# Optimization experiments

Hardware: AMD Instinct MI355X
Metric: run time of the kernel (lower is better)

Reference implementation:

```python
import jax, jax.numpy as jnp
import numpy as np
from jax import lax

NPOINT, RADIUS, NSAMPLE = 1024, 0.2, 32
EPS = 1e-5

def _fps(xyz, npoint):
    # farthest point sampling, xyz [B,N,3] -> idx [B,npoint]
    B, N, _ = xyz.shape
    def body(carry, _):
        dist, far = carry  # [B,N], [B]
        c = jnp.take_along_axis(xyz, far[:, None, None], axis=1)  # [B,1,3]
        d = jnp.sum((xyz - c) ** 2, -1)
        dist = jnp.minimum(dist, d)
        nxt = jnp.argmax(dist, -1).astype(jnp.int32)
        return (dist, nxt), far
    init = (jnp.full((B, N), 1e10, xyz.dtype), jnp.zeros((B,), jnp.int32))
    _, idx = lax.scan(body, init, None, length=npoint)
    return jnp.transpose(idx)  # [B,npoint]

def _index_points(pts, idx):
    # pts [B,N,C], idx [B,...] int -> [B,...,C]
    return jax.vmap(lambda p, i: p[i])(pts, idx)

def _ball_query(radius, nsample, xyz, new_xyz):
    B, N, _ = xyz.shape
    sqr = (jnp.sum(new_xyz ** 2, -1)[:, :, None] + jnp.sum(xyz ** 2, -1)[:, None, :]
           - 2.0 * jnp.einsum('bsc,bnc->bsn', new_xyz, xyz))  # [B,S,N]
    base = jnp.arange(N, dtype=jnp.int32)[None, None, :]
    idx = jnp.where(sqr > radius ** 2, N, base)
    idx = jnp.sort(idx, -1)[..., :nsample]  # [B,S,K]
    first = idx[..., :1]
    return jnp.where(idx == N, jnp.broadcast_to(first, idx.shape), idx)

def _mlp_bn_relu(x, w, b, g, beta):
    # x [B,C,K,S]; 1x1 conv == channel GEMM; BN uses batch stats (training mode)
    x = jnp.einsum('bcks,oc->boks', x, w) + b[None, :, None, None]
    mu = jnp.mean(x, axis=(0, 2, 3), keepdims=True)
    var = jnp.var(x, axis=(0, 2, 3), keepdims=True)
    x = (x - mu) * lax.rsqrt(var + EPS) * g[None, :, None, None] + beta[None, :, None, None]
    return jax.nn.relu(x)

def setup_inputs() -> dict:
    key = jax.random.key(0)
    ks = jax.random.split(key, 16)
    B, N, D = 16, 4096, 3
    mlp = [64, 64, 128]
    inp = {
        'xyz': jax.random.uniform(ks[0], (B, 3, N), jnp.float32),
        'features': jax.random.normal(ks[1], (B, D, N), jnp.float32),
    }
    last = 3 + D
    for i, c in enumerate(mlp):
        inp[f'w{i}'] = jax.random.normal(ks[2 + 4 * i], (c, last), jnp.float32) * (1.0 / np.sqrt(last))
        inp[f'b{i}'] = jnp.zeros((c,), jnp.float32)
        inp[f'g{i}'] = jnp.ones((c,), jnp.float32)
        inp[f'bt{i}'] = jnp.zeros((c,), jnp.float32)
        last = c
    return inp

def reference(xyz, features, w0, b0, g0, bt0, w1, b1, g1, bt1, w2, b2, g2, bt2):
    xyz_t = jnp.transpose(xyz, (0, 2, 1))        # [B,N,3]
    feat_t = jnp.transpose(features, (0, 2, 1))  # [B,N,D]
    fps_idx = _fps(xyz_t, NPOINT)
    new_xyz = _index_points(xyz_t, fps_idx)      # [B,S,3]
    idx = _ball_query(RADIUS, NSAMPLE, xyz_t, new_xyz)  # [B,S,K]
    grouped_xyz = _index_points(xyz_t, idx) - new_xyz[:, :, None, :]  # [B,S,K,3]
    grouped_feat = _index_points(feat_t, idx)                          # [B,S,K,D]
    x = jnp.concatenate([grouped_xyz, grouped_feat], -1)               # [B,S,K,3+D]
    x = jnp.transpose(x, (0, 3, 2, 1))           # [B,C,K,S]
    for (w, b, g, beta) in ((w0, b0, g0, bt0), (w1, b1, g1, bt1), (w2, b2, g2, bt2)):
        x = _mlp_bn_relu(x, w, b, g, beta)
    new_features = jnp.max(x, axis=2)            # [B,C',S]
    return jnp.transpose(new_xyz, (0, 2, 1)), new_features
```

## Files before the change

kernel.cpp:

```cpp
#include <hip/hip_runtime.h>
#include <hip/hip_bf16.h>
#include <stdint.h>

#define NB 16
#define NPTS 4096
#define NS 1024
#define NK 32
#define NT_COLS (NB*NS*NK)
#define NBUCK 64

typedef __hip_bfloat16 bf16;
typedef __attribute__((ext_vector_type(8))) short short8;
typedef __attribute__((ext_vector_type(4))) float floatx4;

__device__ __forceinline__ unsigned short f2bf_bits(float v) {
  bf16 b = __float2bfloat16(v);
  return *(unsigned short*)&b;
}

__global__ void k_zero(float* __restrict__ p) {
  p[blockIdx.x*256 + threadIdx.x] = 0.f;
}

template<int CTRL, int RM, int BM>
__device__ __forceinline__ float fmax_dpp(float x) {
  int o = __builtin_amdgcn_update_dpp(__float_as_int(x), __float_as_int(x),
                                      CTRL, RM, BM, false);
  return fmaxf(x, __int_as_float(o));
}
template<int CTRL>
__device__ __forceinline__ float add_dpp(float x) {
  int o = __builtin_amdgcn_update_dpp(0, __float_as_int(x), CTRL, 0xF, 0xF, true);
  return __fadd_rn(x, __int_as_float(o));
}

__global__ __launch_bounds__(256) void k_fps(const float* __restrict__ xyz,
                                             float* __restrict__ newxyz,
                                             float* __restrict__ out0) {
  __shared__ float xs[NPTS], ys[NPTS], zs[NPTS];
  __shared__ float selx[NS], sely[NS], selz[NS];
  __shared__ float2 pair[2][4];
  const int b = blockIdx.x;
  const int t = threadIdx.x;
  const float* p = xyz + (size_t)b * 3 * NPTS;
  for (int i = t; i < NPTS; i += 256) {
    xs[i] = p[i];
    ys[i] = p[NPTS + i];
    zs[i] = p[2*NPTS + i];
  }
  __syncthreads();
  float px[16], py[16], pz[16], dist[16];
  const int p0 = t * 16;
  #pragma unroll
  for (int j = 0; j < 16; ++j) {
    px[j]=xs[p0+j]; py[j]=ys[p0+j]; pz[j]=zs[p0+j]; dist[j]=1e10f;
  }
  const int lane = t & 63, wv = t >> 6;
  int cur = 0;
  for (int i = 0; i < NS; ++i) {
    float cx = xs[cur], cy = ys[cur], cz = zs[cur];
    if (t == 0) { selx[i] = cx; sely[i] = cy; selz[i] = cz; }
    if (i == NS-1) break;
    float bv = -1.0f; int bi = p0;
    #pragma unroll
    for (int j = 0; j < 16; ++j) {
      float dx = __fsub_rn(px[j], cx);
      float dy = __fsub_rn(py[j], cy);
      float dz = __fsub_rn(pz[j], cz);
      float d  = __fadd_rn(__fadd_rn(__fmul_rn(dx,dx), __fmul_rn(dy,dy)), __fmul_rn(dz,dz));
      float nd = fminf(dist[j], d);
      dist[j] = nd;
      if (nd > bv) { bv = nd; bi = p0 + j; }
    }
    float x = bv;
    x = fmax_dpp<0x111,0xF,0xF>(x);
    x = fmax_dpp<0x112,0xF,0xF>(x);
    x = fmax_dpp<0x114,0xF,0xF>(x);
    x = fmax_dpp<0x118,0xF,0xF>(x);
    x = fmax_dpp<0x142,0xA,0xF>(x);
    x = fmax_dpp<0x143,0xC,0xF>(x);
    float M = __int_as_float(__builtin_amdgcn_readlane(__float_as_int(x), 63));
    unsigned long long mk = __ballot(bv == M);
    int sl  = (int)__builtin_ctzll(mk);
    int wbi = __builtin_amdgcn_readlane(bi, sl);
    if ((t & 63) == 0) pair[i & 1][wv] = make_float2(M, __int_as_float(wbi));
    __syncthreads();
    const float4* pb = (const float4*)&pair[i & 1][0];
    float4 q01 = pb[0], q23 = pb[1];
    float bestv = q01.x; int besti = __float_as_int(q01.y);
    if (q01.z > bestv) { bestv = q01.z; besti = __float_as_int(q01.w); }
    if (q23.x > bestv) { bestv = q23.x; besti = __float_as_int(q23.y); }
    if (q23.z > bestv) { bestv = q23.z; besti = __float_as_int(q23.w); }
    cur = besti;
  }
  __syncthreads();
  for (int i = t; i < NS; i += 256) {
    float vx = selx[i], vy = sely[i], vz = selz[i];
    size_t q = (size_t)b*3*NS + i;
    out0[q] = vx; out0[q + NS] = vy; out0[q + 2*NS] = vz;
    size_t o = (size_t)(b*NS + i)*3;
    newxyz[o] = vx; newxyz[o+1] = vy; newxyz[o+2] = vz;
  }
}

__global__ __launch_bounds__(256) void k_ballq(const float* __restrict__ xyz,
                                               const float* __restrict__ newxyz,
                                               int* __restrict__ idx) {
  const int gw = (blockIdx.x * 256 + threadIdx.x) >> 6;
  const int lane = threadIdx.x & 63;
  const int b = gw >> 10;
  const int s = gw & (NS-1);
  const float* xb = xyz + (size_t)b * 3 * NPTS;
  const size_t nq = (size_t)(b*NS + s)*3;
  const float nx = newxyz[nq], ny = newxyz[nq+1], nz = newxyz[nq+2];
  const float sn = __fadd_rn(__fadd_rn(__fmul_rn(nx,nx), __fmul_rn(ny,ny)), __fmul_rn(nz,nz));
  const float R2 = (float)(0.2*0.2);
  int* out = idx + (size_t)gw * NK;
  int cnt = 0, first = 0;
  for (int c0 = 0; c0 < NPTS; c0 += 64) {
    int n = c0 + lane;
    float x = xb[n], y = xb[NPTS+n], z = xb[2*NPTS+n];
    float sx = __fadd_rn(__fadd_rn(__fmul_rn(x,x), __fmul_rn(y,y)), __fmul_rn(z,z));
    float dt = __fadd_rn(__fadd_rn(__fmul_rn(nx,x), __fmul_rn(ny,y)), __fmul_rn(nz,z));
    float sqr = __fsub_rn(__fadd_rn(sn, sx), __fmul_rn(2.0f, dt));
    bool inr = (sqr <= R2);
    unsigned long long m = __ballot(inr);
    if (m != 0ull) {
      if (cnt == 0) first = c0 + (int)__builtin_ctzll(m);
      int rank = __popcll(m & ((1ull << lane) - 1ull));
      int pos = cnt + rank;
      if (inr && pos < NK) out[pos] = n;
      cnt += __popcll(m);
      if (cnt >= NK) break;
    }
  }
  int tot = cnt < NK ? cnt : NK;
  if (lane >= tot && lane < NK) out[lane] = first;
}

__global__ __launch_bounds__(256) void k_layer1(const float* __restrict__ xyz,
                                                const float* __restrict__ feat,
                                                const float* __restrict__ newxyz,
                                                const int* __restrict__ idx,
                                                const float* __restrict__ w0,
                                                const float* __restrict__ b0,
                                                bf16* __restrict__ x1) {
  __shared__ float w[64*6];
  __shared__ float bias[64];
  for (int i = threadIdx.x; i < 64*6; i += 256) w[i] = w0[i];
  if (threadIdx.x < 64) bias[threadIdx.x] = b0[threadIdx.x];
  __syncthreads();
  const int col = blockIdx.x * 256 + threadIdx.x;
  const int bs = col >> 5;
  const int b  = bs >> 10;
  const int n  = idx[col];
  const float* xb = xyz  + (size_t)b*3*NPTS;
  const float* fb = feat + (size_t)b*3*NPTS;
  float in[6];
  in[0] = __fsub_rn(xb[n],        newxyz[(size_t)bs*3]);
  in[1] = __fsub_rn(xb[NPTS+n],   newxyz[(size_t)bs*3+1]);
  in[2] = __fsub_rn(xb[2*NPTS+n], newxyz[(size_t)bs*3+2]);
  in[3] = fb[n];
  in[4] = fb[NPTS+n];
  in[5] = fb[2*NPTS+n];
  #pragma unroll
  for (int o = 0; o < 64; ++o) {
    float acc = bias[o];
    #pragma unroll
    for (int c = 0; c < 6; ++c) acc = fmaf(in[c], w[o*6+c], acc);
    x1[(size_t)o*NT_COLS + col] = __float2bfloat16(acc);
  }
}

__global__ __launch_bounds__(256) void k_stats(const bf16* __restrict__ x,
                                               float* __restrict__ accum, int C) {
  const int o = blockIdx.x >> 5;
  const int chunk = blockIdx.x & 31;
  const uint4* p = (const uint4*)(x + (size_t)o*NT_COLS + (size_t)chunk*16384);
  float s = 0.f, ss = 0.f;
  #pragma unroll
  for (int it = 0; it < 8; ++it) {
    uint4 u = p[threadIdx.x + it*256];
    uint32_t wr[4] = {u.x, u.y, u.z, u.w};
    #pragma unroll
    for (int q = 0; q < 4; ++q) {
      float a  = __uint_as_float(wr[q] << 16);
      float bq = __uint_as_float(wr[q] & 0xffff0000u);
      s += a;  ss = fmaf(a, a, ss);
      s += bq; ss = fmaf(bq, bq, ss);
    }
  }
  #pragma unroll
  for (int off = 32; off; off >>= 1) { s += __shfl_xor(s, off); ss += __shfl_xor(ss, off); }
  __shared__ float ls[4], lss[4];
  const int lane = threadIdx.x & 63, wv = threadIdx.x >> 6;
  if (lane == 0) { ls[wv] = s; lss[wv] = ss; }
  __syncthreads();
  if (threadIdx.x == 0) {
    float* dst = accum + (size_t)(blockIdx.x & (NBUCK-1))*(2*C);
    atomicAdd(&dst[o],     (ls[0]+ls[1])+(ls[2]+ls[3]));
    atomicAdd(&dst[C + o], (lss[0]+lss[1])+(lss[2]+lss[3]));
  }
}

__global__ void k_finalize(const float* __restrict__ accum,
                           const float* __restrict__ g, const float* __restrict__ beta,
                           float* __restrict__ scsh, int C) {
  int o = threadIdx.x;
  if (o < C) {
    float s = 0.f, ss = 0.f;
    for (int bkt = 0; bkt < NBUCK; ++bkt) {
      s  += accum[(size_t)bkt*(2*C) + o];
      ss += accum[(size_t)bkt*(2*C) + C + o];
    }
    const float n = (float)NT_COLS;
    float mu  = s / n;
    float var = ss / n - mu*mu;
    if (var < 0.f) var = 0.f;
    float rs = rsqrtf(var + 1e-5f);
    float sc = g[o] * rs;
    scsh[o]   = sc;
    scsh[C+o] = beta[o] - mu * sc;
  }
}

#define XT_STRIDE 72
template<int CO, bool POOL>
__global__ __launch_bounds__(256) void k_layerN_mfma(
    const bf16*  __restrict__ xin,
    const float* __restrict__ wN,
    const float* __restrict__ bN,
    const float* __restrict__ scsh,
    float*       __restrict__ accum,
    bf16*        __restrict__ xout,
    float*       __restrict__ mx) {
  constexpr int RT = CO/16;
  __shared__ short xT[256*XT_STRIDE];
  __shared__ float sc_s[64], sh_s[64], bias_s[CO];
  const int t = threadIdx.x;
  const int col0 = blockIdx.x * 256;
  if (t < 64) { sc_s[t] = scsh[t]; sh_s[t] = scsh[64+t]; }
  if (t < CO) bias_s[t] = bN[t];
  __syncthreads();
  {
    const int col = col0 + t;
    #pragma unroll
    for (int c0 = 0; c0 < 64; c0 += 8) {
      short8 pk;
      #pragma unroll
      for (int j = 0; j < 8; ++j) {
        float v = __bfloat162float(xin[(size_t)(c0+j)*NT_COLS + col]);
        v = fmaxf(fmaf(v, sc_s[c0+j], sh_s[c0+j]), 0.f);
        pk[j] = (short)f2bf_bits(v);
      }
      *((short8*)&xT[t*XT_STRIDE + c0]) = pk;
    }
  }
  __syncthreads();
  const int lane = t & 63, wv = t >> 6;
  const int qd = lane >> 4, ln = lane & 15;
  short8 A[RT][2];
  #pragma unroll
  for (int rt = 0; rt < RT; ++rt) {
    #pragma unroll
    for (int kh = 0; kh < 2; ++kh) {
      const float* wp = wN + (size_t)(rt*16 + ln)*64 + kh*32 + qd*8;
      float4 f0 = *(const float4*)wp;
      float4 f1 = *(const float4*)(wp + 4);
      short8 a;
      a[0]=(short)f2bf_bits(f0.x); a[1]=(short)f2bf_bits(f0.y);
      a[2]=(short)f2bf_bits(f0.z); a[3]=(short)f2bf_bits(f0.w);
      a[4]=(short)f2bf_bits(f1.x); a[5]=(short)f2bf_bits(f1.y);
      a[6]=(short)f2bf_bits(f1.z); a[7]=(short)f2bf_bits(f1.w);
      A[rt][kh] = a;
    }
  }
  floatx4 acc[RT][4];
  #pragma unroll
  for (int rt = 0; rt < RT; ++rt)
    #pragma unroll
    for (int ct = 0; ct < 4; ++ct)
      acc[rt][ct] = (floatx4)0.f;
  #pragma unroll
  for (int ct = 0; ct < 4; ++ct) {
    const int coll = wv*64 + ct*16 + ln;
    short8 B0 = *((const short8*)&xT[coll*XT_STRIDE + qd*8]);
    short8 B1 = *((const short8*)&xT[coll*XT_STRIDE + 32 + qd*8]);
    #pragma unroll
    for (int rt = 0; rt < RT; ++rt) {
      acc[rt][ct] = __builtin_amdgcn_mfma_f32_16x16x32_bf16(A[rt][0], B0, acc[rt][ct], 0,0,0);
      acc[rt][ct] = __builtin_amdgcn_mfma_f32_16x16x32_bf16(A[rt][1], B1, acc[rt][ct], 0,0,0);
    }
  }
  float* dst = accum + (size_t)(blockIdx.x & (NBUCK-1))*(2*CO);
  const int bs0 = (col0 + wv*64) >> 5;
  #pragma unroll
  for (int rt = 0; rt < RT; ++rt) {
    float s[4]  = {0.f,0.f,0.f,0.f};
    float sq[4] = {0.f,0.f,0.f,0.f};
    float mxv[2][4];
    #pragma unroll
    for (int h = 0; h < 2; ++h)
      #pragma unroll
      for (int r = 0; r < 4; ++r) mxv[h][r] = -3.402823466e38f;
    #pragma unroll
    for (int ct = 0; ct < 4; ++ct) {
      const int col = col0 + wv*64 + ct*16 + ln;
      #pragma unroll
      for (int r = 0; r < 4; ++r) {
        const int o = rt*16 + qd*4 + r;
        float v = acc[rt][ct][r] + bias_s[o];
        if (!POOL) xout[(size_t)o*NT_COLS + col] = __float2bfloat16(v);
        else mxv[ct>>1][r] = fmaxf(mxv[ct>>1][r], v);
        s[r] += v; sq[r] = fmaf(v, v, sq[r]);
      }
    }
    if (POOL) {
      #pragma unroll
      for (int h = 0; h < 2; ++h) {
        #pragma unroll
        for (int r = 0; r < 4; ++r) {
          float m = mxv[h][r];
          m = fmax_dpp<0x111,0xF,0xF>(m);
          m = fmax_dpp<0x112,0xF,0xF>(m);
          m = fmax_dpp<0x114,0xF,0xF>(m);
          m = fmax_dpp<0x118,0xF,0xF>(m);
          if (ln == 15) {
            const int o = rt*16 + qd*4 + r;
            mx[(size_t)o*(NT_COLS/NK) + bs0 + h] = m;
          }
        }
      }
    }
    #pragma unroll
    for (int r = 0; r < 4; ++r) {
      float a = s[r], q = sq[r];
      a = add_dpp<0x111>(a); a = add_dpp<0x112>(a);
      a = add_dpp<0x114>(a); a = add_dpp<0x118>(a);
      q = add_dpp<0x111>(q); q = add_dpp<0x112>(q);
      q = add_dpp<0x114>(q); q = add_dpp<0x118>(q);
      if (ln == 15) {
        const int o = rt*16 + qd*4 + r;
        atomicAdd(&dst[o], a);
        atomicAdd(&dst[CO + o], q);
      }
    }
  }
}

__global__ __launch_bounds__(256) void k_bnmax(const float* __restrict__ mx,
                                               const float* __restrict__ scsh,
                                               float* __restrict__ out1) {
  const int blk = blockIdx.x;
  const int o = blk & 127;
  const int b = blk >> 7;
  const float sc = scsh[o], sh = scsh[128+o];
  const int s = threadIdx.x * 4;
  float4 v = *(const float4*)(mx + (size_t)o*(NT_COLS/NK) + b*NS + s);
  float4 r;
  r.x = fmaxf(fmaf(v.x, sc, sh), 0.f);
  r.y = fmaxf(fmaf(v.y, sc, sh), 0.f);
  r.z = fmaxf(fmaf(v.z, sc, sh), 0.f);
  r.w = fmaxf(fmaf(v.w, sc, sh), 0.f);
  *(float4*)(out1 + (size_t)(b*128 + o)*NS + s) = r;
}

extern "C" void kernel_launch(void* const* d_in, const int* in_sizes, int n_in,
                              void* d_out, int out_size, void* d_ws, size_t ws_size,
                              hipStream_t stream) {
  const float* xyz  = (const float*)d_in[0];
  const float* feat = (const float*)d_in[1];
  const float* w0 = (const float*)d_in[2];
  const float* b0 = (const float*)d_in[3];
  const float* g0 = (const float*)d_in[4];
  const float* bt0= (const float*)d_in[5];
  const float* w1 = (const float*)d_in[6];
  const float* b1 = (const float*)d_in[7];
  const float* g1 = (const float*)d_in[8];
  const float* bt1= (const float*)d_in[9];
  const float* w2 = (const float*)d_in[10];
  const float* b2 = (const float*)d_in[11];
  const float* g2 = (const float*)d_in[12];
  const float* bt2= (const float*)d_in[13];

  float* out0 = (float*)d_out;
  float* out1 = out0 + (size_t)NB*3*NS;

  char* ws = (char*)d_ws;
  float* accum  = (float*)(ws + 0);
  float* acc_l1 = accum;
  float* acc_l2 = accum + 8192;
  float* acc_l3 = accum + 16384;
  float* scsh   = (float*)(ws + 131072);
  float* newxyz = (float*)(ws + 133120);
  int*   bidx   = (int*)  (ws + 329728);
  bf16*  x2     = (bf16*) (ws + 2426880);
  bf16*  x1     = (bf16*) (ws + 69535744);
  float* mx3    = (float*)(ws + 136644608);

  k_zero <<<128, 256, 0, stream>>>(accum);

  k_fps  <<<NB,   256, 0, stream>>>(xyz, newxyz, out0);
  k_ballq<<<16384/4, 256, 0, stream>>>(xyz, newxyz, bidx);
  k_layer1<<<NT_COLS/256, 256, 0, stream>>>(xyz, feat, newxyz, bidx, w0, b0, x1);

  k_stats   <<<64*32, 256, 0, stream>>>(x1, acc_l1, 64);
  k_finalize<<<1,     256, 0, stream>>>(acc_l1, g0, bt0, scsh + 0, 64);

  k_layerN_mfma<64,false><<<NT_COLS/256, 256, 0, stream>>>(x1, w1, b1, scsh + 0, acc_l2, x2, nullptr);
  k_finalize<<<1,     256, 0, stream>>>(acc_l2, g1, bt1, scsh + 128, 64);

  k_layerN_mfma<128,true><<<NT_COLS/256, 256, 0, stream>>>(x2, w2, b2, scsh + 128, acc_l3, nullptr, mx3);
  k_finalize<<<1,     256, 0, stream>>>(acc_l3, g2, bt2, scsh + 256, 128);

  k_bnmax <<<NB*128, 256, 0, stream>>>(mx3, scsh + 256, out1);
}
```

Measured before the change: 908.9 us.

## Fuse layer-1 BN statistics into layer1 kernel and carry FPS centroid coordinates

Drops the separate k_stats pass over the bf16 layer-1 activations. Per-channel sum and sum-of-squares are now computed inside k_layer1 with a 64-lane DPP reduction and atomics into the bucketed accumulator. Statistics now come from the fp32 values rather than the rounded bf16 ones. In FPS, the winning lane writes its candidate's xyz directly into the shared pair slot, which removes the readlane of the index and the dependent shared-memory lookup on the serial per-iteration path. The fused kernel issues 64 extra reductions per wave and many atomics per block.

After: 1.073 ms. +18.1%, slower.

```diff
diff --git a/kernel.cpp b/kernel.cpp
--- a/kernel.cpp
+++ b/kernel.cpp
@@ -28,10 +28,22 @@
                                       CTRL, RM, BM, false);
   return fmaxf(x, __int_as_float(o));
 }
-template<int CTRL>
+template<int CTRL, int RM>
 __device__ __forceinline__ float add_dpp(float x) {
-  int o = __builtin_amdgcn_update_dpp(0, __float_as_int(x), CTRL, 0xF, 0xF, true);
+  int o = __builtin_amdgcn_update_dpp(0, __float_as_int(x), CTRL, RM, 0xF, true);
   return __fadd_rn(x, __int_as_float(o));
+}
+__device__ __forceinline__ float add16_dpp(float x) {
+  x = add_dpp<0x111,0xF>(x); x = add_dpp<0x112,0xF>(x);
+  x = add_dpp<0x114,0xF>(x); x = add_dpp<0x118,0xF>(x);
+  return x;
+}
+__device__ __forceinline__ float add64_dpp(float x) {
+  x = add_dpp<0x111,0xF>(x); x = add_dpp<0x112,0xF>(x);
+  x = add_dpp<0x114,0xF>(x); x = add_dpp<0x118,0xF>(x);
+  x = add_dpp<0x142,0xA>(x);
+  x = add_dpp<0x143,0xC>(x);
+  return x;
 }
 
 __global__ __launch_bounds__(256) void k_fps(const float* __restrict__ xyz,
@@ -39,7 +51,7 @@
                                              float* __restrict__ out0) {
   __shared__ float xs[NPTS], ys[NPTS], zs[NPTS];
   __shared__ float selx[NS], sely[NS], selz[NS];
-  __shared__ float2 pair[2][4];
+  __shared__ float4 pair[2][4];
   const int b = blockIdx.x;
   const int t = threadIdx.x;
   const float* p = xyz + (size_t)b * 3 * NPTS;
@@ -56,9 +68,8 @@
     px[j]=xs[p0+j]; py[j]=ys[p0+j]; pz[j]=zs[p0+j]; dist[j]=1e10f;
   }
   const int lane = t & 63, wv = t >> 6;
-  int cur = 0;
+  float cx = xs[0], cy = ys[0], cz = zs[0];
   for (int i = 0; i < NS; ++i) {
-    float cx = xs[cur], cy = ys[cur], cz = zs[cur];
     if (t == 0) { selx[i] = cx; sely[i] = cy; selz[i] = cz; }
     if (i == NS-1) break;
     float bv = -1.0f; int bi = p0;
@@ -72,6 +83,7 @@
       dist[j] = nd;
       if (nd > bv) { bv = nd; bi = p0 + j; }
     }
+    float candx = xs[bi], candy = ys[bi], candz = zs[bi];
     float x = bv;
     x = fmax_dpp<0x111,0xF,0xF>(x);
     x = fmax_dpp<0x112,0xF,0xF>(x);
@@ -81,17 +93,18 @@
     x = fmax_dpp<0x143,0xC,0xF>(x);
     float M = __int_as_float(__builtin_amdgcn_readlane(__float_as_int(x), 63));
     unsigned long long mk = __ballot(bv == M);
-    int sl  = (int)__builtin_ctzll(mk);
-    int wbi = __builtin_amdgcn_readlane(bi, sl);
-    if ((t & 63) == 0) pair[i & 1][wv] = make_float2(M, __int_as_float(wbi));
+    int sl = (int)__builtin_ctzll(mk);
+    if (lane == sl) pair[i & 1][wv] = make_float4(M, candx, candy, candz);
     __syncthreads();
-    const float4* pb = (const float4*)&pair[i & 1][0];
-    float4 q01 = pb[0], q23 = pb[1];
-    float bestv = q01.x; int besti = __float_as_int(q01.y);
-    if (q01.z > bestv) { bestv = q01.z; besti = __float_as_int(q01.w); }
-    if (q23.x > bestv) { bestv = q23.x; besti = __float_as_int(q23.y); }
-    if (q23.z > bestv) { bestv = q23.z; besti = __float_as_int(q23.w); }
-    cur = besti;
+    float4 q0 = pair[i & 1][0];
+    float4 q1 = pair[i & 1][1];
+    float4 q2 = pair[i & 1][2];
+    float4 q3 = pair[i & 1][3];
+    float bestv = q0.x; float wx = q0.y, wy = q0.z, wz = q0.w;
+    if (q1.x > bestv) { bestv = q1.x; wx = q1.y; wy = q1.z; wz = q1.w; }
+    if (q2.x > bestv) { bestv = q2.x; wx = q2.y; wy = q2.z; wz = q2.w; }
+    if (q3.x > bestv) { bestv = q3.x; wx = q3.y; wy = q3.z; wz = q3.w; }
+    cx = wx; cy = wy; cz = wz;
   }
   __syncthreads();
   for (int i = t; i < NS; i += 256) {
@@ -144,6 +157,7 @@
                                                 const int* __restrict__ idx,
                                                 const float* __restrict__ w0,
                                                 const float* __restrict__ b0,
+                                                float* __restrict__ accum,
                                                 bf16* __restrict__ x1) {
   __shared__ float w[64*6];
   __shared__ float bias[64];
@@ -163,43 +177,20 @@
   in[3] = fb[n];
   in[4] = fb[NPTS+n];
   in[5] = fb[2*NPTS+n];
+  const int lane = threadIdx.x & 63;
+  float* dst = accum + (size_t)(blockIdx.x & (NBUCK-1))*128;
   #pragma unroll
   for (int o = 0; o < 64; ++o) {
     float acc = bias[o];
     #pragma unroll
     for (int c = 0; c < 6; ++c) acc = fmaf(in[c], w[o*6+c], acc);
     x1[(size_t)o*NT_COLS + col] = __float2bfloat16(acc);
-  }
-}
-
-__global__ __launch_bounds__(256) void k_stats(const bf16* __restrict__ x,
-                                               float* __restrict__ accum, int C) {
-  const int o = blockIdx.x >> 5;
-  const int chunk = blockIdx.x & 31;
-  const uint4* p = (const uint4*)(x + (size_t)o*NT_COLS + (size_t)chunk*16384);
-  float s = 0.f, ss = 0.f;
-  #pragma unroll
-  for (int it = 0; it < 8; ++it) {
-    uint4 u = p[threadIdx.x + it*256];
-    uint32_t wr[4] = {u.x, u.y, u.z, u.w};
-    #pragma unroll
-    for (int q = 0; q < 4; ++q) {
-      float a  = __uint_as_float(wr[q] << 16);
-      float bq = __uint_as_float(wr[q] & 0xffff0000u);
-      s += a;  ss = fmaf(a, a, ss);
-      s += bq; ss = fmaf(bq, bq, ss);
-    }
-  }
-  #pragma unroll
-  for (int off = 32; off; off >>= 1) { s += __shfl_xor(s, off); ss += __shfl_xor(ss, off); }
-  __shared__ float ls[4], lss[4];
-  const int lane = threadIdx.x & 63, wv = threadIdx.x >> 6;
-  if (lane == 0) { ls[wv] = s; lss[wv] = ss; }
-  __syncthreads();
-  if (threadIdx.x == 0) {
-    float* dst = accum + (size_t)(blockIdx.x & (NBUCK-1))*(2*C);
-    atomicAdd(&dst[o],     (ls[0]+ls[1])+(ls[2]+ls[3]));
-    atomicAdd(&dst[C + o], (lss[0]+lss[1])+(lss[2]+lss[3]));
+    float s = add64_dpp(acc);
+    float q = add64_dpp(__fmul_rn(acc, acc));
+    if (lane == 63) {
+      atomicAdd(&dst[o], s);
+      atomicAdd(&dst[64 + o], q);
+    }
   }
 }
 
@@ -334,11 +325,8 @@
     }
     #pragma unroll
     for (int r = 0; r < 4; ++r) {
-      float a = s[r], q = sq[r];
-      a = add_dpp<0x111>(a); a = add_dpp<0x112>(a);
-      a = add_dpp<0x114>(a); a = add_dpp<0x118>(a);
-      q = add_dpp<0x111>(q); q = add_dpp<0x112>(q);
-      q = add_dpp<0x114>(q); q = add_dpp<0x118>(q);
+      float a = add16_dpp(s[r]);
+      float q = add16_dpp(sq[r]);
       if (ln == 15) {
         const int o = rt*16 + qd*4 + r;
         atomicAdd(&dst[o], a);
@@ -402,9 +390,7 @@
 
   k_fps  <<<NB,   256, 0, stream>>>(xyz, newxyz, out0);
   k_ballq<<<16384/4, 256, 0, stream>>>(xyz, newxyz, bidx);
-  k_layer1<<<NT_COLS/256, 256, 0, stream>>>(xyz, feat, newxyz, bidx, w0, b0, x1);
-
-  k_stats   <<<64*32, 256, 0, stream>>>(x1, acc_l1, 64);
+  k_layer1<<<NT_COLS/256, 256, 0, stream>>>(xyz, feat, newxyz, bidx, w0, b0, acc_l1, x1);
   k_finalize<<<1,     256, 0, stream>>>(acc_l1, g0, bt0, scsh + 0, 64);
 
   k_layerN_mfma<64,false><<<NT_COLS/256, 256, 0, stream>>>(x1, w1, b1, scsh + 0, acc_l2, x2, nullptr);
```
